# Performance work log

Hardware: AMD Instinct MI355X
Metric: run time of the kernel (lower is better)

Reference implementation:

```python
import jax, jax.numpy as jnp
import numpy as np

# --- Instant-NGP hashgrid config (from INGP.build_encoding) ---
L = 16            # cfg_model.encoding.levels
F = 2             # cfg_model.encoding.hashgrid.dim
T = 1 << 19       # 2 ** log2_hashmap_size
BASE = 16         # 2 ** min_logres
FINEST = 2048     # 2 ** max_logres
GROWTH = np.exp((np.log(FINEST) - np.log(BASE)) / (L - 1))
RES = np.floor(BASE * GROWTH ** np.arange(L)).astype(np.float32)  # per-level resolution
VMIN, VMAX = -1.0, 1.0  # voxel_range
N_POINTS = 524288

# 8 trilinear corner offsets, and NGP spatial-hash primes
CORNERS = np.array([[i, j, k] for i in (0, 1) for j in (0, 1) for k in (0, 1)],
                   dtype=np.uint32)                       # [8,3]
PRIMES = np.array([1, 2654435761, 805459861], dtype=np.uint32)


def setup_inputs() -> dict:
    key = jax.random.key(0)
    k1, k2 = jax.random.split(key)
    points_3D = jax.random.uniform(k1, (N_POINTS, 3), minval=-1.0, maxval=1.0,
                                   dtype=jnp.float32)
    # torch-ngp 'uniform' init: U(-1e-4, 1e-4)
    tables = jax.random.uniform(k2, (L, T, F), minval=-1e-4, maxval=1e-4,
                                dtype=jnp.float32)
    return {"points_3D": points_3D, "tables": tables}


def _hash_encode(x, tables):
    """x: [N,3] in [0,1]; tables: [L,T,F] -> [N, L*F]."""
    corners_u = jnp.asarray(CORNERS)            # [8,3] uint32
    corners_b = jnp.asarray(CORNERS.astype(bool))
    p0u, p1u, p2u = (jnp.uint32(int(p)) for p in PRIMES)
    mask = jnp.uint32(T - 1)

    def level(table, r):
        pos = x * r                              # [N,3]
        p0 = jnp.floor(pos)
        w = pos - p0                             # trilinear weights [N,3]
        c = p0.astype(jnp.uint32)[:, None, :] + corners_u[None]  # [N,8,3]
        h = (c[..., 0] * p0u) ^ (c[..., 1] * p1u) ^ (c[..., 2] * p2u)
        idx = (h & mask).astype(jnp.int32)       # [N,8] hashed bucket ids
        vals = table[idx]                        # [N,8,F] irregular gather
        wc = jnp.where(corners_b[None], w[:, None, :], 1.0 - w[:, None, :]).prod(-1)
        return jnp.einsum('nc,ncf->nf', wc, vals)  # [N,F]

    feats = jax.vmap(level)(tables, jnp.asarray(RES))  # [L,N,F]
    n = x.shape[0]
    return jnp.transpose(feats, (1, 0, 2)).reshape(n, L * F)


def reference(points_3D, tables):
    # _encode_3D with contract=False: normalize to [0,1] over voxel_range
    x = (points_3D - VMIN) / (VMAX - VMIN)
    feat = _hash_encode(x, tables)
    return feat.astype(jnp.float32)
```

## Files before the change

### kernel.cpp

```cpp
#include <hip/hip_runtime.h>
#include <cmath>


constexpr int LVLS = 16;
constexpr unsigned TBL = 1u << 19;
constexpr unsigned TMASK = TBL - 1u;
constexpr unsigned P1 = 2654435761u;
constexpr unsigned P2 = 805459861u;
constexpr int PTS_PER_BLOCK = 512;

typedef float vf2 __attribute__((ext_vector_type(2)));
typedef float vf4 __attribute__((ext_vector_type(4)));

struct ResArr { float r[LVLS]; };

template<bool USE_WS>
__global__ __launch_bounds__(256) void ingp_gather(
    const float* __restrict__ pts,
    const float* __restrict__ tables,
    float2* __restrict__ dst,
    ResArr ra, int npts, int bpl)
{
    __shared__ float s_res[LVLS];
    __shared__ float s_pts[PTS_PER_BLOCK * 3];
    if (threadIdx.x < LVLS) s_res[threadIdx.x] = ra.r[threadIdx.x];

    int b = blockIdx.x;
    int phase_blocks = 8 * bpl;
    int xcd = b & 7;
    int phase = b / phase_blocks;
    int lvl = phase == 0 ? xcd : 15 - xcd;
    int q = (b % phase_blocks) >> 3;
    int t = threadIdx.x;

    {
        int base_dw = q * PTS_PER_BLOCK * 3;
        int total_dw = npts * 3 - base_dw;
        const float* src = pts + base_dw;
        #pragma unroll
        for (int k = 0; k < 6; ++k) {
            int i = t + k * 256;
            float v = 0.f;
            if (i < total_dw) v = __builtin_nontemporal_load(src + i);
            s_pts[i] = v;
        }
    }
    __syncthreads();

    float r = s_res[lvl];
    const float2* __restrict__ tab = (const float2*)tables + (size_t)lvl * TBL;

    int p0 = q * PTS_PER_BLOCK + t;

    #pragma unroll
    for (int s = 0; s < 2; ++s) {
        int lp = t + s * 256;
        int pglob = p0 + s * 256;
        bool valid = pglob < npts;
        float px = s_pts[lp * 3 + 0];
        float py = s_pts[lp * 3 + 1];
        float pz = s_pts[lp * 3 + 2];
        float x = (px + 1.0f) * 0.5f;
        float y = (py + 1.0f) * 0.5f;
        float z = (pz + 1.0f) * 0.5f;
        float posx = x * r, posy = y * r, posz = z * r;
        float fx = floorf(posx), fy = floorf(posy), fz = floorf(posz);
        float wx = posx - fx, wy = posy - fy, wz = posz - fz;
        unsigned ix = (unsigned)fx, iy = (unsigned)fy, iz = (unsigned)fz;
        unsigned hx0 = ix,      hx1 = ix + 1u;
        unsigned hy0 = iy * P1, hy1 = hy0 + P1;
        unsigned hz0 = iz * P2, hz1 = hz0 + P2;

        unsigned hyz[4];
        hyz[0] = hy0 ^ hz0;
        hyz[1] = hy0 ^ hz1;
        hyz[2] = hy1 ^ hz0;
        hyz[3] = hy1 ^ hz1;

        float2 v[8];
        if ((ix & 1u) == 0u) {
            #pragma unroll
            for (int yz = 0; yz < 4; ++yz) {
                unsigned b0 = (hx0 ^ hyz[yz]) & TMASK;
                const vf4* lp4 = (const vf4*)(tab + (b0 & ~1u));
                vf4 qd = *lp4;
                float2 lo = make_float2(qd.x, qd.y);
                float2 hi = make_float2(qd.z, qd.w);
                bool odd = (b0 & 1u) != 0u;
                v[yz]     = odd ? hi : lo;
                v[4 + yz] = odd ? lo : hi;
            }
        } else {
            #pragma unroll
            for (int yz = 0; yz < 4; ++yz) {
                unsigned b0 = (hx0 ^ hyz[yz]) & TMASK;
                unsigned b1 = (hx1 ^ hyz[yz]) & TMASK;
                v[yz]     = tab[b0];
                v[4 + yz] = tab[b1];
            }
        }

        float ox = 1.0f - wx, oy = 1.0f - wy, oz = 1.0f - wz;
        float w[8];
        w[0] = (ox * oy) * oz;
        w[1] = (ox * oy) * wz;
        w[2] = (ox * wy) * oz;
        w[3] = (ox * wy) * wz;
        w[4] = (wx * oy) * oz;
        w[5] = (wx * oy) * wz;
        w[6] = (wx * wy) * oz;
        w[7] = (wx * wy) * wz;

        float f0 = w[0] * v[0].x;
        float f1 = w[0] * v[0].y;
        #pragma unroll
        for (int c = 1; c < 8; ++c) {
            f0 += w[c] * v[c].x;
            f1 += w[c] * v[c].y;
        }
        if (valid) {
            vf2 o; o.x = f0; o.y = f1;
            if (USE_WS)
                __builtin_nontemporal_store(o, (vf2*)(dst + (size_t)lvl * npts + pglob));
            else
                dst[(size_t)pglob * LVLS + lvl] = make_float2(f0, f1);
        }
    }
}

__global__ __launch_bounds__(256) void ingp_transpose(
    const float2* __restrict__ ws, float4* __restrict__ out, int npts)
{
    __shared__ float2 a[LVLS][258];
    int base = blockIdx.x * 256;
    int t = threadIdx.x;

    #pragma unroll
    for (int l = 0; l < LVLS; ++l) {
        int pp = base + t;
        float2 val = make_float2(0.f, 0.f);
        if (pp < npts) {
            vf2 v = __builtin_nontemporal_load((const vf2*)(ws + (size_t)l * npts + pp));
            val = make_float2(v.x, v.y);
        }
        a[l][t] = val;
    }
    __syncthreads();

    int j = t & 7;
    int pl = t >> 3;
    #pragma unroll
    for (int it = 0; it < 8; ++it) {
        int pt = pl + it * 32;
        if (base + pt < npts) {
            float2 u = a[2 * j][pt];
            float2 v = a[2 * j + 1][pt];
            vf4 o; o.x = u.x; o.y = u.y; o.z = v.x; o.w = v.y;
            __builtin_nontemporal_store(o, (vf4*)(out + (size_t)(base + pt) * 8 + j));
        }
    }
}

extern "C" void kernel_launch(void* const* d_in, const int* in_sizes, int n_in,
                              void* d_out, int out_size, void* d_ws, size_t ws_size,
                              hipStream_t stream) {
    const float* pts    = (const float*)d_in[0];
    const float* tables = (const float*)d_in[1];
    int npts = in_sizes[0] / 3;

    ResArr ra;
    double growth = exp((log(2048.0) - log(16.0)) / 15.0);
    for (int l = 0; l < LVLS; ++l)
        ra.r[l] = (float)floor(16.0 * pow(growth, (double)l));

    int bpl = (npts + PTS_PER_BLOCK - 1) / PTS_PER_BLOCK;
    int grid = LVLS * bpl;

    size_t ws_needed = (size_t)LVLS * npts * sizeof(float2);
    bool use_ws = ws_size >= ws_needed;

    if (use_ws) {
        float2* ws = (float2*)d_ws;
        hipLaunchKernelGGL(ingp_gather<true>, dim3(grid), dim3(256), 0, stream,
                           pts, tables, ws, ra, npts, bpl);
        hipLaunchKernelGGL(ingp_transpose, dim3((npts + 255) / 256), dim3(256), 0, stream,
                           ws, (float4*)d_out, npts);
    } else {
        hipLaunchKernelGGL(ingp_gather<false>, dim3(grid), dim3(256), 0, stream,
                           pts, tables, (float2*)d_out, ra, npts, bpl);
    }
}
```

Baseline: 312.4 us.

## Prebuild dense blocked tables for coarse levels to replace hashed gathers

Adds a prep kernel that, for the five coarsest levels, gathers hashed table entries into a dense 2x2x2-blocked grid stored in the workspace. The main gather then reads these levels with vectorised, spatially local loads instead of scattered hash lookups. This trades an extra small kernel and more workspace for better cache locality and fewer memory transactions on the coarse levels. Hashed levels are unchanged and the dense path only runs when the workspace is large enough.

```diff
diff --git a/kernel.cpp b/kernel.cpp
--- a/kernel.cpp
+++ b/kernel.cpp
@@ -3,6 +3,7 @@
 
 
 constexpr int LVLS = 16;
+constexpr int NDENSE = 5;
 constexpr unsigned TBL = 1u << 19;
 constexpr unsigned TMASK = TBL - 1u;
 constexpr unsigned P1 = 2654435761u;
@@ -12,18 +13,52 @@
 typedef float vf2 __attribute__((ext_vector_type(2)));
 typedef float vf4 __attribute__((ext_vector_type(4)));
 
-struct ResArr { float r[LVLS]; };
+struct LvlCfg {
+    float r[LVLS];
+    int doff[LVLS];
+    int dBy[LVLS];
+    int dBz[LVLS];
+};
+
+__global__ __launch_bounds__(256) void ingp_prep(
+    const float* __restrict__ tables, float2* __restrict__ dense,
+    LvlCfg cfg, int total)
+{
+    int i = blockIdx.x * 256 + threadIdx.x;
+    if (i >= total) return;
+    int l = 0, off = cfg.doff[0], By = cfg.dBy[0], Bz = cfg.dBz[0];
+    #pragma unroll
+    for (int k = 1; k < NDENSE; ++k)
+        if (i >= cfg.doff[k]) { l = k; off = cfg.doff[k]; By = cfg.dBy[k]; Bz = cfg.dBz[k]; }
+    int e = i - off;
+    int sub = e & 7, blk = e >> 3;
+    int bz = blk % Bz; int tmp = blk / Bz;
+    int by = tmp % By; int bx = tmp / By;
+    unsigned cx = (unsigned)(bx * 2 + ((sub >> 2) & 1));
+    unsigned cy = (unsigned)(by * 2 + ((sub >> 1) & 1));
+    unsigned cz = (unsigned)(bz * 2 + (sub & 1));
+    unsigned h = cx ^ (cy * P1) ^ (cz * P2);
+    const float2* tab = (const float2*)tables + (size_t)l * TBL;
+    dense[i] = tab[h & TMASK];
+}
 
 template<bool USE_WS>
 __global__ __launch_bounds__(256) void ingp_gather(
     const float* __restrict__ pts,
     const float* __restrict__ tables,
+    const float2* __restrict__ dense,
     float2* __restrict__ dst,
-    ResArr ra, int npts, int bpl)
+    LvlCfg cfg, int npts, int bpl, int ndense)
 {
     __shared__ float s_res[LVLS];
+    __shared__ int s_doff[LVLS], s_dBy[LVLS], s_dBz[LVLS];
     __shared__ float s_pts[PTS_PER_BLOCK * 3];
-    if (threadIdx.x < LVLS) s_res[threadIdx.x] = ra.r[threadIdx.x];
+    if (threadIdx.x < LVLS) {
+        s_res[threadIdx.x]  = cfg.r[threadIdx.x];
+        s_doff[threadIdx.x] = cfg.doff[threadIdx.x];
+        s_dBy[threadIdx.x]  = cfg.dBy[threadIdx.x];
+        s_dBz[threadIdx.x]  = cfg.dBz[threadIdx.x];
+    }
 
     int b = blockIdx.x;
     int phase_blocks = 8 * bpl;
@@ -48,7 +83,11 @@
     __syncthreads();
 
     float r = s_res[lvl];
+    bool dense_lvl = lvl < ndense;
     const float2* __restrict__ tab = (const float2*)tables + (size_t)lvl * TBL;
+    const float2* __restrict__ dtab = dense + (dense_lvl ? s_doff[lvl] : 0);
+    unsigned By = dense_lvl ? (unsigned)s_dBy[lvl] : 1u;
+    unsigned Bz = dense_lvl ? (unsigned)s_dBz[lvl] : 1u;
 
     int p0 = q * PTS_PER_BLOCK + t;
 
@@ -67,36 +106,76 @@
         float fx = floorf(posx), fy = floorf(posy), fz = floorf(posz);
         float wx = posx - fx, wy = posy - fy, wz = posz - fz;
         unsigned ix = (unsigned)fx, iy = (unsigned)fy, iz = (unsigned)fz;
-        unsigned hx0 = ix,      hx1 = ix + 1u;
-        unsigned hy0 = iy * P1, hy1 = hy0 + P1;
-        unsigned hz0 = iz * P2, hz1 = hz0 + P2;
-
-        unsigned hyz[4];
-        hyz[0] = hy0 ^ hz0;
-        hyz[1] = hy0 ^ hz1;
-        hyz[2] = hy1 ^ hz0;
-        hyz[3] = hy1 ^ hz1;
 
         float2 v[8];
-        if ((ix & 1u) == 0u) {
-            #pragma unroll
-            for (int yz = 0; yz < 4; ++yz) {
-                unsigned b0 = (hx0 ^ hyz[yz]) & TMASK;
-                const vf4* lp4 = (const vf4*)(tab + (b0 & ~1u));
-                vf4 qd = *lp4;
-                float2 lo = make_float2(qd.x, qd.y);
-                float2 hi = make_float2(qd.z, qd.w);
-                bool odd = (b0 & 1u) != 0u;
-                v[yz]     = odd ? hi : lo;
-                v[4 + yz] = odd ? lo : hi;
+
+        if (dense_lvl) {
+            unsigned bx0 = ix >> 1, pxb = ix & 1u;
+            unsigned by0 = iy >> 1, pyb = iy & 1u;
+            unsigned bz0 = iz >> 1, pzb = iz & 1u;
+            unsigned rx0 = bx0 * By;
+            unsigned rx1 = (bx0 + pxb) * By;
+            unsigned r00 = (rx0 + by0) * Bz;
+            unsigned r01 = (rx0 + by0 + pyb) * Bz;
+            unsigned r10 = (rx1 + by0) * Bz;
+            unsigned r11 = (rx1 + by0 + pyb) * Bz;
+            unsigned x0 = pxb * 4u, x1 = 4u - x0;
+            unsigned y0 = pyb * 2u, y1 = 2u - y0;
+            unsigned s00 = x0 + y0, s01 = x0 + y1, s10 = x1 + y0, s11 = x1 + y1;
+            if (pzb == 0u) {
+                unsigned e00 = (r00 + bz0) * 8u + s00;
+                unsigned e01 = (r01 + bz0) * 8u + s01;
+                unsigned e10 = (r10 + bz0) * 8u + s10;
+                unsigned e11 = (r11 + bz0) * 8u + s11;
+                vf4 q0 = *(const vf4*)(dtab + e00);
+                vf4 q1 = *(const vf4*)(dtab + e01);
+                vf4 q2 = *(const vf4*)(dtab + e10);
+                vf4 q3 = *(const vf4*)(dtab + e11);
+                v[0] = make_float2(q0.x, q0.y); v[1] = make_float2(q0.z, q0.w);
+                v[2] = make_float2(q1.x, q1.y); v[3] = make_float2(q1.z, q1.w);
+                v[4] = make_float2(q2.x, q2.y); v[5] = make_float2(q2.z, q2.w);
+                v[6] = make_float2(q3.x, q3.y); v[7] = make_float2(q3.z, q3.w);
+            } else {
+                unsigned bzA = bz0, bzB = bz0 + 1u;
+                v[0] = dtab[(r00 + bzA) * 8u + s00 + 1u];
+                v[1] = dtab[(r00 + bzB) * 8u + s00];
+                v[2] = dtab[(r01 + bzA) * 8u + s01 + 1u];
+                v[3] = dtab[(r01 + bzB) * 8u + s01];
+                v[4] = dtab[(r10 + bzA) * 8u + s10 + 1u];
+                v[5] = dtab[(r10 + bzB) * 8u + s10];
+                v[6] = dtab[(r11 + bzA) * 8u + s11 + 1u];
+                v[7] = dtab[(r11 + bzB) * 8u + s11];
             }
         } else {
-            #pragma unroll
-            for (int yz = 0; yz < 4; ++yz) {
-                unsigned b0 = (hx0 ^ hyz[yz]) & TMASK;
-                unsigned b1 = (hx1 ^ hyz[yz]) & TMASK;
-                v[yz]     = tab[b0];
-                v[4 + yz] = tab[b1];
+            unsigned hx0 = ix,      hx1 = ix + 1u;
+            unsigned hy0 = iy * P1;
+            unsigned hz0 = iz * P2, hz1 = hz0 + P2;
+            unsigned hyz[4];
+            hyz[0] = hy0 ^ hz0;
+            hyz[1] = hy0 ^ hz1;
+            hyz[2] = (hy0 + P1) ^ hz0;
+            hyz[3] = (hy0 + P1) ^ hz1;
+
+            if ((ix & 1u) == 0u) {
+                #pragma unroll
+                for (int yz = 0; yz < 4; ++yz) {
+                    unsigned b0 = (hx0 ^ hyz[yz]) & TMASK;
+                    const vf4* lp4 = (const vf4*)(tab + (b0 & ~1u));
+                    vf4 qd = *lp4;
+                    float2 lo = make_float2(qd.x, qd.y);
+                    float2 hi = make_float2(qd.z, qd.w);
+                    bool odd = (b0 & 1u) != 0u;
+                    v[yz]     = odd ? hi : lo;
+                    v[4 + yz] = odd ? lo : hi;
+                }
+            } else {
+                #pragma unroll
+                for (int yz = 0; yz < 4; ++yz) {
+                    unsigned b0 = (hx0 ^ hyz[yz]) & TMASK;
+                    unsigned b1 = (hx1 ^ hyz[yz]) & TMASK;
+                    v[yz]     = tab[b0];
+                    v[4 + yz] = tab[b1];
+                }
             }
         }
 
@@ -168,25 +247,46 @@
     const float* tables = (const float*)d_in[1];
     int npts = in_sizes[0] / 3;
 
-    ResArr ra;
+    LvlCfg cfg;
     double growth = exp((log(2048.0) - log(16.0)) / 15.0);
-    for (int l = 0; l < LVLS; ++l)
-        ra.r[l] = (float)floor(16.0 * pow(growth, (double)l));
+    int cum = 0;
+    for (int l = 0; l < LVLS; ++l) {
+        cfg.r[l] = (float)floor(16.0 * pow(growth, (double)l));
+        cfg.doff[l] = 0; cfg.dBy[l] = 1; cfg.dBz[l] = 1;
+        if (l < NDENSE) {
+            int R = (int)cfg.r[l] + 1;
+            int B = (R + 1) >> 1;
+            cfg.doff[l] = cum;
+            cfg.dBy[l] = B; cfg.dBz[l] = B;
+            cum += 8 * B * B * B;
+        }
+    }
+    size_t dense_bytes = (size_t)cum * sizeof(float2);
 
     int bpl = (npts + PTS_PER_BLOCK - 1) / PTS_PER_BLOCK;
     int grid = LVLS * bpl;
 
     size_t ws_needed = (size_t)LVLS * npts * sizeof(float2);
     bool use_ws = ws_size >= ws_needed;
+    bool use_dense = use_ws && (ws_size >= ws_needed + dense_bytes);
+
+    float2* dense = use_dense ? (float2*)((char*)d_ws + ws_needed) : nullptr;
+    int ndense = use_dense ? NDENSE : 0;
+
+    if (use_dense) {
+        int pgrid = (cum + 255) / 256;
+        hipLaunchKernelGGL(ingp_prep, dim3(pgrid), dim3(256), 0, stream,
+                           tables, dense, cfg, cum);
+    }
 
     if (use_ws) {
         float2* ws = (float2*)d_ws;
         hipLaunchKernelGGL(ingp_gather<true>, dim3(grid), dim3(256), 0, stream,
-                           pts, tables, ws, ra, npts, bpl);
+                           pts, tables, dense, ws, cfg, npts, bpl, ndense);
         hipLaunchKernelGGL(ingp_transpose, dim3((npts + 255) / 256), dim3(256), 0, stream,
                            ws, (float4*)d_out, npts);
     } else {
         hipLaunchKernelGGL(ingp_gather<false>, dim3(grid), dim3(256), 0, stream,
-                           pts, tables, (float2*)d_out, ra, npts, bpl);
-    }
-}
+                           pts, tables, dense, (float2*)d_out, cfg, npts, bpl, ndense);
+    }
+}
```

Result: slower. 319.4 us (+2.3%).

## Precompute dense z-pair tables for coarse levels to cut gather transactions

Applied to the files above, without the earlier changes.

Adds a prep kernel that, on every call, materialises the hashed table entries of the five coarsest levels into a dense grid. Each cell holds its own entry and its z+1 neighbour packed together, so a point on those levels needs four 16-byte loads at computed addresses instead of hashed scattered loads. The dense grid is written into the output buffer, which the transpose kernel overwrites afterwards. The change also vectorises the point staging loads for full blocks and simplifies the odd-ix hashed path. It adds an extra kernel launch and extra memory traffic, and relies on the output buffer being large enough to hold the dense grid.

```diff
diff --git a/kernel.cpp b/kernel.cpp
--- a/kernel.cpp
+++ b/kernel.cpp
@@ -3,6 +3,7 @@
 
 
 constexpr int LVLS = 16;
+constexpr int NDENSE = 5;
 constexpr unsigned TBL = 1u << 19;
 constexpr unsigned TMASK = TBL - 1u;
 constexpr unsigned P1 = 2654435761u;
@@ -12,18 +13,54 @@
 typedef float vf2 __attribute__((ext_vector_type(2)));
 typedef float vf4 __attribute__((ext_vector_type(4)));
 
-struct ResArr { float r[LVLS]; };
+struct LvlCfg {
+    float r[LVLS];
+    int doff[LVLS];
+    int dZ[LVLS];
+    int dXZ[LVLS];
+};
+
+__global__ __launch_bounds__(256) void ingp_prep(
+    const float* __restrict__ tables, vf4* __restrict__ dense,
+    LvlCfg cfg, int total)
+{
+    int i = blockIdx.x * 256 + threadIdx.x;
+    if (i >= total) return;
+    int l = 0;
+    #pragma unroll
+    for (int k = 1; k < NDENSE; ++k) if (i >= cfg.doff[k]) l = k;
+    int e = i - cfg.doff[l];
+    int Z = cfg.dZ[l];
+    int X = cfg.dXZ[l] / Z;
+    int z = e % Z; int t2 = e / Z;
+    int y = t2 % X; int x = t2 / X;
+    unsigned hy = (unsigned)y * P1;
+    unsigned hz = (unsigned)z * P2;
+    unsigned h0 = ((unsigned)x ^ hy ^ hz) & TMASK;
+    unsigned h1 = ((unsigned)x ^ hy ^ (hz + P2)) & TMASK;
+    const float2* tab = (const float2*)tables + (size_t)l * TBL;
+    float2 a = tab[h0], b = tab[h1];
+    vf4 o; o.x = a.x; o.y = a.y; o.z = b.x; o.w = b.y;
+    __builtin_nontemporal_store(o, dense + i);
+}
 
 template<bool USE_WS>
 __global__ __launch_bounds__(256) void ingp_gather(
     const float* __restrict__ pts,
     const float* __restrict__ tables,
+    const vf4* __restrict__ dense,
     float2* __restrict__ dst,
-    ResArr ra, int npts, int bpl)
+    LvlCfg cfg, int npts, int bpl, int ndense)
 {
     __shared__ float s_res[LVLS];
+    __shared__ int s_doff[LVLS], s_dZ[LVLS], s_dXZ[LVLS];
     __shared__ float s_pts[PTS_PER_BLOCK * 3];
-    if (threadIdx.x < LVLS) s_res[threadIdx.x] = ra.r[threadIdx.x];
+    if (threadIdx.x < LVLS) {
+        s_res[threadIdx.x]  = cfg.r[threadIdx.x];
+        s_doff[threadIdx.x] = cfg.doff[threadIdx.x];
+        s_dZ[threadIdx.x]   = cfg.dZ[threadIdx.x];
+        s_dXZ[threadIdx.x]  = cfg.dXZ[threadIdx.x];
+    }
 
     int b = blockIdx.x;
     int phase_blocks = 8 * bpl;
@@ -37,18 +74,34 @@
         int base_dw = q * PTS_PER_BLOCK * 3;
         int total_dw = npts * 3 - base_dw;
         const float* src = pts + base_dw;
-        #pragma unroll
-        for (int k = 0; k < 6; ++k) {
-            int i = t + k * 256;
-            float v = 0.f;
-            if (i < total_dw) v = __builtin_nontemporal_load(src + i);
-            s_pts[i] = v;
+        if (total_dw >= PTS_PER_BLOCK * 3) {
+            const vf4* src4 = (const vf4*)src;
+            #pragma unroll
+            for (int k = 0; k < 2; ++k) {
+                int i4 = t + k * 256;
+                if (i4 < PTS_PER_BLOCK * 3 / 4) {
+                    vf4 v = __builtin_nontemporal_load(src4 + i4);
+                    *(vf4*)(s_pts + i4 * 4) = v;
+                }
+            }
+        } else {
+            #pragma unroll
+            for (int k = 0; k < 6; ++k) {
+                int i = t + k * 256;
+                float v = 0.f;
+                if (i < total_dw) v = __builtin_nontemporal_load(src + i);
+                s_pts[i] = v;
+            }
         }
     }
     __syncthreads();
 
     float r = s_res[lvl];
+    bool dense_lvl = lvl < ndense;
     const float2* __restrict__ tab = (const float2*)tables + (size_t)lvl * TBL;
+    const vf4* __restrict__ dtab = dense_lvl ? dense + s_doff[lvl] : (const vf4*)tab;
+    unsigned Z  = dense_lvl ? (unsigned)s_dZ[lvl]  : 1u;
+    unsigned XZ = dense_lvl ? (unsigned)s_dXZ[lvl] : 1u;
 
     int p0 = q * PTS_PER_BLOCK + t;
 
@@ -67,36 +120,42 @@
         float fx = floorf(posx), fy = floorf(posy), fz = floorf(posz);
         float wx = posx - fx, wy = posy - fy, wz = posz - fz;
         unsigned ix = (unsigned)fx, iy = (unsigned)fy, iz = (unsigned)fz;
-        unsigned hx0 = ix,      hx1 = ix + 1u;
-        unsigned hy0 = iy * P1, hy1 = hy0 + P1;
-        unsigned hz0 = iz * P2, hz1 = hz0 + P2;
-
-        unsigned hyz[4];
-        hyz[0] = hy0 ^ hz0;
-        hyz[1] = hy0 ^ hz1;
-        hyz[2] = hy1 ^ hz0;
-        hyz[3] = hy1 ^ hz1;
 
         float2 v[8];
-        if ((ix & 1u) == 0u) {
+
+        if (dense_lvl) {
+            unsigned e00 = ix * XZ + iy * Z + iz;
+            vf4 q00 = dtab[e00];
+            vf4 q01 = dtab[e00 + Z];
+            vf4 q10 = dtab[e00 + XZ];
+            vf4 q11 = dtab[e00 + XZ + Z];
+            v[0] = make_float2(q00.x, q00.y); v[1] = make_float2(q00.z, q00.w);
+            v[2] = make_float2(q01.x, q01.y); v[3] = make_float2(q01.z, q01.w);
+            v[4] = make_float2(q10.x, q10.y); v[5] = make_float2(q10.z, q10.w);
+            v[6] = make_float2(q11.x, q11.y); v[7] = make_float2(q11.z, q11.w);
+        } else {
+            unsigned hy0 = iy * P1;
+            unsigned hz0 = iz * P2;
+            unsigned hyz[4];
+            hyz[0] = hy0 ^ hz0;
+            hyz[1] = hy0 ^ (hz0 + P2);
+            hyz[2] = (hy0 + P1) ^ hz0;
+            hyz[3] = (hy0 + P1) ^ (hz0 + P2);
+
             #pragma unroll
             for (int yz = 0; yz < 4; ++yz) {
-                unsigned b0 = (hx0 ^ hyz[yz]) & TMASK;
-                const vf4* lp4 = (const vf4*)(tab + (b0 & ~1u));
-                vf4 qd = *lp4;
+                unsigned b0 = (ix ^ hyz[yz]) & TMASK;
+                vf4 qd = *(const vf4*)(tab + (b0 & ~1u));
                 float2 lo = make_float2(qd.x, qd.y);
                 float2 hi = make_float2(qd.z, qd.w);
                 bool odd = (b0 & 1u) != 0u;
                 v[yz]     = odd ? hi : lo;
                 v[4 + yz] = odd ? lo : hi;
             }
-        } else {
-            #pragma unroll
-            for (int yz = 0; yz < 4; ++yz) {
-                unsigned b0 = (hx0 ^ hyz[yz]) & TMASK;
-                unsigned b1 = (hx1 ^ hyz[yz]) & TMASK;
-                v[yz]     = tab[b0];
-                v[4 + yz] = tab[b1];
+            if (ix & 1u) {
+                #pragma unroll
+                for (int yz = 0; yz < 4; ++yz)
+                    v[4 + yz] = tab[((ix + 1u) ^ hyz[yz]) & TMASK];
             }
         }
 
@@ -168,25 +227,47 @@
     const float* tables = (const float*)d_in[1];
     int npts = in_sizes[0] / 3;
 
-    ResArr ra;
+    LvlCfg cfg;
     double growth = exp((log(2048.0) - log(16.0)) / 15.0);
-    for (int l = 0; l < LVLS; ++l)
-        ra.r[l] = (float)floor(16.0 * pow(growth, (double)l));
+    int cum = 0;
+    for (int l = 0; l < LVLS; ++l) {
+        cfg.r[l] = (float)floor(16.0 * pow(growth, (double)l));
+        cfg.doff[l] = 0; cfg.dZ[l] = 1; cfg.dXZ[l] = 1;
+        if (l < NDENSE) {
+            int R = (int)cfg.r[l];
+            int X = R + 2;
+            int Z = R + 1;
+            cfg.doff[l] = cum;
+            cfg.dZ[l] = Z; cfg.dXZ[l] = X * Z;
+            cum += X * X * Z;
+        }
+    }
+    size_t dense_bytes = (size_t)cum * 16;
 
     int bpl = (npts + PTS_PER_BLOCK - 1) / PTS_PER_BLOCK;
     int grid = LVLS * bpl;
 
     size_t ws_needed = (size_t)LVLS * npts * sizeof(float2);
     bool use_ws = ws_size >= ws_needed;
+    bool use_dense = use_ws && ((size_t)out_size >= dense_bytes);
+
+    vf4* dense = use_dense ? (vf4*)d_out : nullptr;
+    int ndense = use_dense ? NDENSE : 0;
+
+    if (use_dense) {
+        int pgrid = (cum + 255) / 256;
+        hipLaunchKernelGGL(ingp_prep, dim3(pgrid), dim3(256), 0, stream,
+                           tables, dense, cfg, cum);
+    }
 
     if (use_ws) {
         float2* ws = (float2*)d_ws;
         hipLaunchKernelGGL(ingp_gather<true>, dim3(grid), dim3(256), 0, stream,
-                           pts, tables, ws, ra, npts, bpl);
+                           pts, tables, dense, ws, cfg, npts, bpl, ndense);
         hipLaunchKernelGGL(ingp_transpose, dim3((npts + 255) / 256), dim3(256), 0, stream,
                            ws, (float4*)d_out, npts);
     } else {
         hipLaunchKernelGGL(ingp_gather<false>, dim3(grid), dim3(256), 0, stream,
-                           pts, tables, (float2*)d_out, ra, npts, bpl);
-    }
-}
+                           pts, tables, dense, (float2*)d_out, cfg, npts, bpl, ndense);
+    }
+}
```

New measurement: 356.1 us. 1.14x slower.

## Spatially sort points by Morton bin before hash-grid gather

Applied to the files above, without the earlier changes.

Adds a counting sort of points into 32^3 Morton-ordered bins (histogram, single-block scan, atomic scatter), using the output buffer as scratch for the sorted points. The gather then visits spatially nearby points together, which should improve cache locality of table lookups at coarse levels. The transpose writes results back through the permutation. The block-to-level mapping is also changed to run the fine levels first, and point loads now use vector reads. The cost is several extra kernel launches, atomics, and a scattered output write pattern.

```diff
diff --git a/kernel.cpp b/kernel.cpp
--- a/kernel.cpp
+++ b/kernel.cpp
@@ -8,11 +8,75 @@
 constexpr unsigned P1 = 2654435761u;
 constexpr unsigned P2 = 805459861u;
 constexpr int PTS_PER_BLOCK = 512;
+constexpr int NBINS = 32768;
 
 typedef float vf2 __attribute__((ext_vector_type(2)));
 typedef float vf4 __attribute__((ext_vector_type(4)));
 
 struct ResArr { float r[LVLS]; };
+
+__device__ __forceinline__ unsigned spread5(unsigned v) {
+    v &= 31u;
+    v = (v | (v << 8)) & 0x100Fu;
+    v = (v | (v << 4)) & 0x10C3u;
+    v = (v | (v << 2)) & 0x1249u;
+    return v;
+}
+
+__device__ __forceinline__ unsigned bin_key(float px, float py, float pz) {
+    float x = (px + 1.0f) * 0.5f;
+    float y = (py + 1.0f) * 0.5f;
+    float z = (pz + 1.0f) * 0.5f;
+    unsigned bx = (unsigned)fminf(31.f, fmaxf(0.f, floorf(x * 32.f)));
+    unsigned by = (unsigned)fminf(31.f, fmaxf(0.f, floorf(y * 32.f)));
+    unsigned bz = (unsigned)fminf(31.f, fmaxf(0.f, floorf(z * 32.f)));
+    return spread5(bx) | (spread5(by) << 1) | (spread5(bz) << 2);
+}
+
+__global__ __launch_bounds__(256) void ingp_hist(
+    const float* __restrict__ pts, unsigned* __restrict__ hist, int npts)
+{
+    int i = blockIdx.x * 256 + threadIdx.x;
+    if (i >= npts) return;
+    float px = pts[i * 3 + 0], py = pts[i * 3 + 1], pz = pts[i * 3 + 2];
+    atomicAdd(&hist[bin_key(px, py, pz)], 1u);
+}
+
+__global__ __launch_bounds__(1024) void ingp_scan(
+    const unsigned* __restrict__ hist, unsigned* __restrict__ offs)
+{
+    __shared__ unsigned sc[1024];
+    int t = threadIdx.x;
+    unsigned loc[32];
+    unsigned s = 0;
+    #pragma unroll
+    for (int i = 0; i < 32; ++i) { loc[i] = s; s += hist[t * 32 + i]; }
+    sc[t] = s;
+    __syncthreads();
+    for (int d = 1; d < 1024; d <<= 1) {
+        unsigned v = (t >= d) ? sc[t - d] : 0u;
+        __syncthreads();
+        sc[t] += v;
+        __syncthreads();
+    }
+    unsigned base = sc[t] - s;
+    #pragma unroll
+    for (int i = 0; i < 32; ++i) offs[t * 32 + i] = base + loc[i];
+}
+
+__global__ __launch_bounds__(256) void ingp_scatter(
+    const float* __restrict__ pts, unsigned* __restrict__ offs,
+    float* __restrict__ pts_s, int* __restrict__ perm, int npts)
+{
+    int i = blockIdx.x * 256 + threadIdx.x;
+    if (i >= npts) return;
+    float px = pts[i * 3 + 0], py = pts[i * 3 + 1], pz = pts[i * 3 + 2];
+    unsigned pos = atomicAdd(&offs[bin_key(px, py, pz)], 1u);
+    pts_s[pos * 3 + 0] = px;
+    pts_s[pos * 3 + 1] = py;
+    pts_s[pos * 3 + 2] = pz;
+    perm[pos] = i;
+}
 
 template<bool USE_WS>
 __global__ __launch_bounds__(256) void ingp_gather(
@@ -26,23 +90,33 @@
     if (threadIdx.x < LVLS) s_res[threadIdx.x] = ra.r[threadIdx.x];
 
     int b = blockIdx.x;
-    int phase_blocks = 8 * bpl;
-    int xcd = b & 7;
-    int phase = b / phase_blocks;
-    int lvl = phase == 0 ? xcd : 15 - xcd;
-    int q = (b % phase_blocks) >> 3;
+    int lvl, q;
+    if (b < 8 * bpl) { lvl = 8 + (b & 7); q = b >> 3; }
+    else { int u = b - 8 * bpl; lvl = u / bpl; q = u - lvl * bpl; }
     int t = threadIdx.x;
 
     {
         int base_dw = q * PTS_PER_BLOCK * 3;
         int total_dw = npts * 3 - base_dw;
         const float* src = pts + base_dw;
-        #pragma unroll
-        for (int k = 0; k < 6; ++k) {
-            int i = t + k * 256;
-            float v = 0.f;
-            if (i < total_dw) v = __builtin_nontemporal_load(src + i);
-            s_pts[i] = v;
+        if (total_dw >= PTS_PER_BLOCK * 3) {
+            const vf4* src4 = (const vf4*)src;
+            #pragma unroll
+            for (int k = 0; k < 2; ++k) {
+                int i4 = t + k * 256;
+                if (i4 < PTS_PER_BLOCK * 3 / 4) {
+                    vf4 v = __builtin_nontemporal_load(src4 + i4);
+                    *(vf4*)(s_pts + i4 * 4) = v;
+                }
+            }
+        } else {
+            #pragma unroll
+            for (int k = 0; k < 6; ++k) {
+                int i = t + k * 256;
+                float v = 0.f;
+                if (i < total_dw) v = __builtin_nontemporal_load(src + i);
+                s_pts[i] = v;
+            }
         }
     }
     __syncthreads();
@@ -68,14 +142,14 @@
         float wx = posx - fx, wy = posy - fy, wz = posz - fz;
         unsigned ix = (unsigned)fx, iy = (unsigned)fy, iz = (unsigned)fz;
         unsigned hx0 = ix,      hx1 = ix + 1u;
-        unsigned hy0 = iy * P1, hy1 = hy0 + P1;
+        unsigned hy0 = iy * P1;
         unsigned hz0 = iz * P2, hz1 = hz0 + P2;
 
         unsigned hyz[4];
         hyz[0] = hy0 ^ hz0;
         hyz[1] = hy0 ^ hz1;
-        hyz[2] = hy1 ^ hz0;
-        hyz[3] = hy1 ^ hz1;
+        hyz[2] = (hy0 + P1) ^ hz0;
+        hyz[3] = (hy0 + P1) ^ hz1;
 
         float2 v[8];
         if ((ix & 1u) == 0u) {
@@ -129,11 +203,15 @@
 }
 
 __global__ __launch_bounds__(256) void ingp_transpose(
-    const float2* __restrict__ ws, float4* __restrict__ out, int npts)
+    const float2* __restrict__ ws, const int* __restrict__ perm,
+    float4* __restrict__ out, int npts)
 {
     __shared__ float2 a[LVLS][258];
+    __shared__ int s_perm[256];
     int base = blockIdx.x * 256;
     int t = threadIdx.x;
+
+    if (base + t < npts) s_perm[t] = perm ? perm[base + t] : base + t;
 
     #pragma unroll
     for (int l = 0; l < LVLS; ++l) {
@@ -153,10 +231,11 @@
     for (int it = 0; it < 8; ++it) {
         int pt = pl + it * 32;
         if (base + pt < npts) {
+            int orig = s_perm[pt];
             float2 u = a[2 * j][pt];
             float2 v = a[2 * j + 1][pt];
             vf4 o; o.x = u.x; o.y = u.y; o.z = v.x; o.w = v.y;
-            __builtin_nontemporal_store(o, (vf4*)(out + (size_t)(base + pt) * 8 + j));
+            __builtin_nontemporal_store(o, (vf4*)(out + (size_t)orig * 8 + j));
         }
     }
 }
@@ -177,14 +256,37 @@
     int grid = LVLS * bpl;
 
     size_t ws_needed = (size_t)LVLS * npts * sizeof(float2);
+    size_t sort_extra = (size_t)npts * sizeof(int) + 2ull * NBINS * sizeof(unsigned);
     bool use_ws = ws_size >= ws_needed;
-
-    if (use_ws) {
+    bool use_sort = use_ws && (ws_size >= ws_needed + sort_extra)
+                           && ((size_t)out_size >= (size_t)npts * 3 * sizeof(float));
+
+    int pgrid = (npts + 255) / 256;
+
+    if (use_sort) {
+        float2*  ws    = (float2*)d_ws;
+        int*     perm  = (int*)((char*)d_ws + ws_needed);
+        unsigned* hist = (unsigned*)(perm + npts);
+        unsigned* offs = hist + NBINS;
+        float*   pts_s = (float*)d_out;
+
+        hipMemsetAsync(hist, 0, NBINS * sizeof(unsigned), stream);
+        hipLaunchKernelGGL(ingp_hist, dim3(pgrid), dim3(256), 0, stream,
+                           pts, hist, npts);
+        hipLaunchKernelGGL(ingp_scan, dim3(1), dim3(1024), 0, stream,
+                           hist, offs);
+        hipLaunchKernelGGL(ingp_scatter, dim3(pgrid), dim3(256), 0, stream,
+                           pts, offs, pts_s, perm, npts);
+        hipLaunchKernelGGL(ingp_gather<true>, dim3(grid), dim3(256), 0, stream,
+                           pts_s, tables, ws, ra, npts, bpl);
+        hipLaunchKernelGGL(ingp_transpose, dim3(pgrid), dim3(256), 0, stream,
+                           ws, perm, (float4*)d_out, npts);
+    } else if (use_ws) {
         float2* ws = (float2*)d_ws;
         hipLaunchKernelGGL(ingp_gather<true>, dim3(grid), dim3(256), 0, stream,
                            pts, tables, ws, ra, npts, bpl);
-        hipLaunchKernelGGL(ingp_transpose, dim3((npts + 255) / 256), dim3(256), 0, stream,
-                           ws, (float4*)d_out, npts);
+        hipLaunchKernelGGL(ingp_transpose, dim3(pgrid), dim3(256), 0, stream,
+                           ws, (const int*)nullptr, (float4*)d_out, npts);
     } else {
         hipLaunchKernelGGL(ingp_gather<false>, dim3(grid), dim3(256), 0, stream,
                            pts, tables, (float2*)d_out, ra, npts, bpl);
```

New measurement: 324.9 us. +4.0%, slower.
